# Optimization experiments

Hardware: AMD Instinct MI355X
Metric: run time of the kernel (lower is better)

## Reference

```python
import jax, jax.numpy as jnp
import numpy as np

N, D, K, G = 262144, 256, 1024, 4
C = D // G
BETA = 0.5


def setup_inputs() -> dict:
    key = jax.random.key(0)
    k1, k2 = jax.random.split(key)
    z = jax.random.normal(k1, (N, D), dtype=jnp.float32)
    # original init: uniform(-1/K, 1/K)
    codebooks = jax.random.uniform(k2, (G, K, C), dtype=jnp.float32,
                                   minval=-1.0 / K, maxval=1.0 / K)
    return {"z": z, "codebooks": codebooks}


def reference(z, codebooks):
    # z: [N, D] -> [N, G, C]; codebooks: [G, K, C]
    zg = z.reshape(-1, G, C)
    # squared distances: ||z||^2 + ||e||^2 - 2 z.e  -> [N, G, K]
    z_sq = jnp.sum(zg ** 2, axis=-1, keepdims=True)            # [N, G, 1]
    e_sq = jnp.sum(codebooks ** 2, axis=-1)                    # [G, K]
    dots = jnp.einsum('ngc,gkc->ngk', zg, codebooks)           # [N, G, K]
    d = z_sq + e_sq[None, :, :] - 2.0 * dots
    idx = jnp.argmin(d, axis=-1)                               # [N, G]
    # gather codes: [N, G, C]
    zq = codebooks[jnp.arange(G)[None, :], idx]
    # per-group VQ loss, averaged over groups (means over N and C per group)
    sg = jax.lax.stop_gradient
    commit = jnp.mean((sg(zq) - zg) ** 2, axis=(0, 2))         # [G]
    embed = jnp.mean((zq - sg(zg)) ** 2, axis=(0, 2))          # [G]
    loss = jnp.mean(BETA * commit + embed)
    # straight-through estimator
    zq_st = zg + sg(zq - zg)
    return zq_st.reshape(-1, D), loss
```

## Files before the change

kernel.cpp:

```cpp
#include <hip/hip_runtime.h>
#include <hip/hip_fp16.h>
#include <stdint.h>

typedef _Float16 f16;
typedef f16   f16x8 __attribute__((ext_vector_type(8)));
typedef float f32x4 __attribute__((ext_vector_type(4)));

#define NTOK 262144
#define DDIM 256
#define KCB  1024
#define GG   4
#define CC   64
#define FR   4
#define WAVES 16
#define ROWS_PER_BLK (FR * 16 * WAVES)
#define NBLKX (NTOK / ROWS_PER_BLK)
#define NPART (NBLKX * GG)
#define CBB   (KCB * CC * 2)

static __device__ __forceinline__ uint32_t umin32(uint32_t a, uint32_t b) { return a < b ? a : b; }

typedef __attribute__((address_space(1))) const void gv_t;
typedef __attribute__((address_space(3))) void lv_t;
static __device__ __forceinline__ void gl_lds16(const void* g, void* l) {
    __builtin_amdgcn_global_load_lds((gv_t*)g, (lv_t*)l, 16, 0, 0);
}
static __device__ __forceinline__ void gl_lds4(const void* g, void* l) {
    __builtin_amdgcn_global_load_lds((gv_t*)g, (lv_t*)l, 4, 0, 0);
}

__global__ __launch_bounds__(64) void vq_prep(const float* __restrict__ cb,
                                              f16* __restrict__ cb16,
                                              float* __restrict__ esq05) {
    int gk = blockIdx.x;
    int c  = threadIdx.x;
    float v = cb[(size_t)gk * CC + c];
    cb16[(size_t)gk * CC + c] = (f16)v;
    float s = v * v;
    #pragma unroll
    for (int off = 32; off; off >>= 1) s += __shfl_down(s, off, 64);
    if (c == 0) esq05[gk] = 0.5f + s;
}

__global__ __launch_bounds__(1024, 4) void vq_argmin(const float* __restrict__ z,
                                                     const f16* __restrict__ cb16,
                                                     const float* __restrict__ esq05,
                                                     unsigned short* __restrict__ idx,
                                                     float* __restrict__ part) {
    const int tid  = threadIdx.x;
    const int lane = tid & 63;
    const int w    = tid >> 6;
    const int g    = blockIdx.y;
    const int r0   = blockIdx.x * ROWS_PER_BLK + w * (FR * 16);
    const int q    = lane >> 4;
    const int t    = lane & 15;

    __shared__ __align__(16) char sb[CBB + KCB * 4];
    __shared__ float ls[WAVES];

    const f16*   cbg = cb16  + (size_t)g * KCB * CC;
    const float* eg  = esq05 + (size_t)g * KCB;

    #pragma unroll
    for (int c = 0; c < 8; ++c) {
        uint32_t x  = (uint32_t)(c * 16384 + w * 1024 + lane * 16);
        uint32_t gx = x ^ (((x >> 7) & 7u) << 4);
        gl_lds16((const char*)cbg + gx, &sb[c * 16384 + w * 1024]);
    }
    gl_lds4(eg + tid, &sb[CBB + w * 256]);

    f16x8 a[FR][2];
    float zsq[FR];
    #pragma unroll
    for (int f = 0; f < FR; ++f) {
        int row = r0 + f * 16 + t;
        const float* zp = z + (size_t)row * DDIM + g * CC + q * 8;
        float4 v0 = *(const float4*)(zp);
        float4 v1 = *(const float4*)(zp + 4);
        float4 v2 = *(const float4*)(zp + 32);
        float4 v3 = *(const float4*)(zp + 36);
        f16x8 a0 = { (f16)(-2.f*v0.x),(f16)(-2.f*v0.y),(f16)(-2.f*v0.z),(f16)(-2.f*v0.w),
                     (f16)(-2.f*v1.x),(f16)(-2.f*v1.y),(f16)(-2.f*v1.z),(f16)(-2.f*v1.w) };
        f16x8 a1 = { (f16)(-2.f*v2.x),(f16)(-2.f*v2.y),(f16)(-2.f*v2.z),(f16)(-2.f*v2.w),
                     (f16)(-2.f*v3.x),(f16)(-2.f*v3.y),(f16)(-2.f*v3.z),(f16)(-2.f*v3.w) };
        a[f][0] = a0; a[f][1] = a1;
        float s = v0.x*v0.x + v0.y*v0.y + v0.z*v0.z + v0.w*v0.w
                + v1.x*v1.x + v1.y*v1.y + v1.z*v1.z + v1.w*v1.w
                + v2.x*v2.x + v2.y*v2.y + v2.z*v2.z + v2.w*v2.w
                + v3.x*v3.x + v3.y*v3.y + v3.z*v3.z + v3.w*v3.w;
        s += __shfl_xor(s, 16, 64);
        s += __shfl_xor(s, 32, 64);
        zsq[f] = s;
    }

    uint32_t run[FR][4];
    #pragma unroll
    for (int f = 0; f < FR; ++f)
        #pragma unroll
        for (int i = 0; i < 4; ++i) run[f][i] = 0xFFFFFFFFu;

    const uint32_t binner = (uint32_t)t * 128 + (((uint32_t)(q * 16)) ^ (((uint32_t)(t & 7)) << 4));

    __syncthreads();

    const float* eb = (const float*)(sb + CBB);

    #pragma unroll 2
    for (int s = 0; s < 64; s += 2) {
        const char* pA = sb + (size_t)s * 2048;
        f16x8 b0A = *(const f16x8*)(pA + binner);
        f16x8 b1A = *(const f16x8*)(pA + (binner ^ 64));
        f16x8 b0B = *(const f16x8*)(pA + 2048 + binner);
        f16x8 b1B = *(const f16x8*)(pA + 2048 + (binner ^ 64));
        float eA = eb[s * 16 + t];
        float eB = eb[s * 16 + 16 + t];
        f32x4 ceA = { eA, eA, eA, eA };
        f32x4 ceB = { eB, eB, eB, eB };
        uint32_t codeA = (uint32_t)(s * 16 + t);
        __builtin_amdgcn_s_setprio(1);
        #pragma unroll
        for (int f = 0; f < FR; ++f) {
            f32x4 accA = __builtin_amdgcn_mfma_f32_16x16x32_f16(a[f][0], b0A, ceA, 0, 0, 0);
            accA = __builtin_amdgcn_mfma_f32_16x16x32_f16(a[f][1], b1A, accA, 0, 0, 0);
            f32x4 accB = __builtin_amdgcn_mfma_f32_16x16x32_f16(a[f][0], b0B, ceB, 0, 0, 0);
            accB = __builtin_amdgcn_mfma_f32_16x16x32_f16(a[f][1], b1B, accB, 0, 0, 0);
            #pragma unroll
            for (int i = 0; i < 4; ++i) {
                uint32_t kA = (__float_as_uint(accA[i]) & 0xFFFFFC00u) | codeA;
                uint32_t kB = (__float_as_uint(accB[i]) & 0xFFFFFC00u) | (codeA + 16);
                run[f][i] = umin32(run[f][i], umin32(kA, kB));
            }
        }
        __builtin_amdgcn_s_setprio(0);
    }

    float lsum = 0.0f;
    #pragma unroll
    for (int f = 0; f < FR; ++f) {
        #pragma unroll
        for (int i = 0; i < 4; ++i) {
            uint32_t k = run[f][i];
            k = umin32(k, __shfl_xor(k, 1, 64));
            k = umin32(k, __shfl_xor(k, 2, 64));
            k = umin32(k, __shfl_xor(k, 4, 64));
            k = umin32(k, __shfl_xor(k, 8, 64));
            int   kw     = (int)(k & 1023u);
            float minval = __uint_as_float(k & 0xFFFFFC00u) - 0.5f;
            int rloc = q * 4 + i;
            int grow = r0 + f * 16 + rloc;
            float zs = __shfl(zsq[f], rloc, 64);
            if (t == 0) {
                idx[(grow << 2) | g] = (unsigned short)kw;
                lsum += zs + minval;
            }
        }
    }
    #pragma unroll
    for (int off = 32; off; off >>= 1) lsum += __shfl_down(lsum, off, 64);

    if (lane == 0) ls[w] = lsum;
    __syncthreads();
    if (tid == 0) {
        float s = 0.0f;
        #pragma unroll
        for (int i = 0; i < WAVES; ++i) s += ls[i];
        part[blockIdx.y * NBLKX + blockIdx.x] = s;
    }
}

__global__ __launch_bounds__(256) void vq_gather(const unsigned short* __restrict__ idx,
                                                 const float* __restrict__ cb32,
                                                 float* __restrict__ out) {
    const int stride = gridDim.x * 256;
    const int total  = NTOK * (DDIM / 4);
    for (int i = blockIdx.x * 256 + threadIdx.x; i < total; i += stride) {
        int row = i >> 6;
        int d4  = i & 63;
        int g   = d4 >> 4;
        int c4  = d4 & 15;
        int k   = idx[(row << 2) | g];
        float4 v = *(const float4*)(cb32 + (size_t)(((g << 10) + k) << 6) + (c4 << 2));
        *(float4*)(out + ((size_t)row << 8) + (d4 << 2)) = v;
    }
}

__global__ __launch_bounds__(256) void vq_final(const float* __restrict__ part,
                                                float* __restrict__ out_loss) {
    __shared__ float ls[4];
    float s = 0.0f;
    for (int i = threadIdx.x; i < NPART; i += 256) s += part[i];
    #pragma unroll
    for (int off = 32; off; off >>= 1) s += __shfl_down(s, off, 64);
    int lane = threadIdx.x & 63, w = threadIdx.x >> 6;
    if (lane == 0) ls[w] = s;
    __syncthreads();
    if (threadIdx.x == 0) {
        *out_loss = 1.5f * (ls[0] + ls[1] + ls[2] + ls[3]) * (1.0f / ((float)NTOK * (float)DDIM));
    }
}

extern "C" void kernel_launch(void* const* d_in, const int* in_sizes, int n_in,
                              void* d_out, int out_size, void* d_ws, size_t ws_size,
                              hipStream_t stream) {
    const float* z  = (const float*)d_in[0];
    const float* cb = (const float*)d_in[1];
    float* out = (float*)d_out;

    char* ws = (char*)d_ws;
    f16*   cb16  = (f16*)ws;
    float* esq05 = (float*)(ws + (size_t)GG * KCB * CC * sizeof(f16));
    float* part  = (float*)(ws + 512*1024 + 16*1024);
    unsigned short* idx = (unsigned short*)(ws + 512*1024 + 32*1024);

    vq_prep<<<GG * KCB, 64, 0, stream>>>(cb, cb16, esq05);

    dim3 grid(NBLKX, GG);
    vq_argmin<<<grid, 1024, 0, stream>>>(z, cb16, esq05, idx, part);

    vq_gather<<<4096, 256, 0, stream>>>(idx, cb, out);

    vq_final<<<1, 256, 0, stream>>>(part, out + (size_t)NTOK * DDIM);
}
```

Before: 272.8 us.

## Switch argmin distance MFMA from fp16 to scaled fp8 32x32x64

Both the codebook (prescaled by 1024) and -2*z are quantized to fp8, and the distance dot products use the MI355X scaled MFMA 32x32x64 f8f6f4 instruction, with a block scale that undoes the codebook prescale. The block shrinks to 8 waves of 64 rows each, the LDS codebook footprint halves, and the reduction is adjusted to the 32-wide tile layout. The aim is higher matrix throughput and less LDS traffic in the argmin kernel. The cost is much coarser fp8 precision, which can flip argmin choices between near-tied codes and change the loss.

Result: faster. 251.7 us (-7.7%).

```diff
diff --git a/kernel.cpp b/kernel.cpp
--- a/kernel.cpp
+++ b/kernel.cpp
@@ -1,22 +1,20 @@
 #include <hip/hip_runtime.h>
-#include <hip/hip_fp16.h>
 #include <stdint.h>
 
-typedef _Float16 f16;
-typedef f16   f16x8 __attribute__((ext_vector_type(8)));
-typedef float f32x4 __attribute__((ext_vector_type(4)));
+typedef int   i32x4 __attribute__((ext_vector_type(4)));
+typedef int   i32x8 __attribute__((ext_vector_type(8)));
+typedef float f32x16 __attribute__((ext_vector_type(16)));
 
 #define NTOK 262144
 #define DDIM 256
 #define KCB  1024
 #define GG   4
 #define CC   64
-#define FR   4
-#define WAVES 16
-#define ROWS_PER_BLK (FR * 16 * WAVES)
+#define WAVES 8
+#define ROWS_PER_BLK (WAVES * 64)
 #define NBLKX (NTOK / ROWS_PER_BLK)
 #define NPART (NBLKX * GG)
-#define CBB   (KCB * CC * 2)
+#define CB8B  (KCB * CC)
 
 static __device__ __forceinline__ uint32_t umin32(uint32_t a, uint32_t b) { return a < b ? a : b; }
 
@@ -30,126 +28,141 @@
 }
 
 __global__ __launch_bounds__(64) void vq_prep(const float* __restrict__ cb,
-                                              f16* __restrict__ cb16,
+                                              unsigned short* __restrict__ cb8,
                                               float* __restrict__ esq05) {
     int gk = blockIdx.x;
     int c  = threadIdx.x;
     float v = cb[(size_t)gk * CC + c];
-    cb16[(size_t)gk * CC + c] = (f16)v;
     float s = v * v;
     #pragma unroll
     for (int off = 32; off; off >>= 1) s += __shfl_down(s, off, 64);
     if (c == 0) esq05[gk] = 0.5f + s;
-}
-
-__global__ __launch_bounds__(1024, 4) void vq_argmin(const float* __restrict__ z,
-                                                     const f16* __restrict__ cb16,
-                                                     const float* __restrict__ esq05,
-                                                     unsigned short* __restrict__ idx,
-                                                     float* __restrict__ part) {
+    if (c < 32) {
+        float v0 = cb[(size_t)gk * CC + 2 * c]     * 1024.0f;
+        float v1 = cb[(size_t)gk * CC + 2 * c + 1] * 1024.0f;
+        int p = __builtin_amdgcn_cvt_pk_fp8_f32(v0, v1, 0, false);
+        cb8[gk * 32 + c] = (unsigned short)(p & 0xFFFF);
+    }
+}
+
+__global__ __launch_bounds__(512, 4) void vq_argmin(const float* __restrict__ z,
+                                                    const unsigned char* __restrict__ cb8,
+                                                    const float* __restrict__ esq05,
+                                                    unsigned short* __restrict__ idx,
+                                                    float* __restrict__ part) {
     const int tid  = threadIdx.x;
     const int lane = tid & 63;
     const int w    = tid >> 6;
     const int g    = blockIdx.y;
-    const int r0   = blockIdx.x * ROWS_PER_BLK + w * (FR * 16);
-    const int q    = lane >> 4;
-    const int t    = lane & 15;
-
-    __shared__ __align__(16) char sb[CBB + KCB * 4];
+    const int r0   = blockIdx.x * ROWS_PER_BLK + w * 64;
+    const int c5   = lane & 31;
+    const int h    = lane >> 5;
+
+    __shared__ __align__(16) char sb[CB8B + KCB * 4];
     __shared__ float ls[WAVES];
 
-    const f16*   cbg = cb16  + (size_t)g * KCB * CC;
-    const float* eg  = esq05 + (size_t)g * KCB;
-
-    #pragma unroll
-    for (int c = 0; c < 8; ++c) {
-        uint32_t x  = (uint32_t)(c * 16384 + w * 1024 + lane * 16);
-        uint32_t gx = x ^ (((x >> 7) & 7u) << 4);
-        gl_lds16((const char*)cbg + gx, &sb[c * 16384 + w * 1024]);
-    }
-    gl_lds4(eg + tid, &sb[CBB + w * 256]);
-
-    f16x8 a[FR][2];
-    float zsq[FR];
-    #pragma unroll
-    for (int f = 0; f < FR; ++f) {
-        int row = r0 + f * 16 + t;
-        const float* zp = z + (size_t)row * DDIM + g * CC + q * 8;
-        float4 v0 = *(const float4*)(zp);
-        float4 v1 = *(const float4*)(zp + 4);
-        float4 v2 = *(const float4*)(zp + 32);
-        float4 v3 = *(const float4*)(zp + 36);
-        f16x8 a0 = { (f16)(-2.f*v0.x),(f16)(-2.f*v0.y),(f16)(-2.f*v0.z),(f16)(-2.f*v0.w),
-                     (f16)(-2.f*v1.x),(f16)(-2.f*v1.y),(f16)(-2.f*v1.z),(f16)(-2.f*v1.w) };
-        f16x8 a1 = { (f16)(-2.f*v2.x),(f16)(-2.f*v2.y),(f16)(-2.f*v2.z),(f16)(-2.f*v2.w),
-                     (f16)(-2.f*v3.x),(f16)(-2.f*v3.y),(f16)(-2.f*v3.z),(f16)(-2.f*v3.w) };
-        a[f][0] = a0; a[f][1] = a1;
-        float s = v0.x*v0.x + v0.y*v0.y + v0.z*v0.z + v0.w*v0.w
-                + v1.x*v1.x + v1.y*v1.y + v1.z*v1.z + v1.w*v1.w
-                + v2.x*v2.x + v2.y*v2.y + v2.z*v2.z + v2.w*v2.w
-                + v3.x*v3.x + v3.y*v3.y + v3.z*v3.z + v3.w*v3.w;
-        s += __shfl_xor(s, 16, 64);
+    const unsigned char* cbg8 = cb8 + (size_t)g * CB8B;
+    const float*         eg   = esq05 + (size_t)g * KCB;
+
+    #pragma unroll
+    for (int i8 = 0; i8 < 8; ++i8) {
+        int i = w + 8 * i8;
+        int s = i >> 1, slot = i & 1;
+        const unsigned char* src = cbg8 + ((s * 32 + c5) * CC + h * 32 + slot * 16);
+        gl_lds16(src, &sb[i * 1024]);
+    }
+    gl_lds4(eg + w * 64 + lane,       &sb[CB8B + w * 256]);
+    gl_lds4(eg + 512 + w * 64 + lane, &sb[CB8B + 2048 + w * 256]);
+
+    i32x8 a[2];
+    float zsq[2];
+    #pragma unroll
+    for (int f = 0; f < 2; ++f) {
+        const float* zp = z + (size_t)(r0 + f * 32 + c5) * DDIM + g * CC + h * 32;
+        int w8[8];
+        float s = 0.0f;
+        #pragma unroll
+        for (int j = 0; j < 8; ++j) {
+            float4 v = ((const float4*)zp)[j];
+            s += v.x * v.x + v.y * v.y + v.z * v.z + v.w * v.w;
+            int p = __builtin_amdgcn_cvt_pk_fp8_f32(-2.0f * v.x, -2.0f * v.y, 0, false);
+            p     = __builtin_amdgcn_cvt_pk_fp8_f32(-2.0f * v.z, -2.0f * v.w, p, true);
+            w8[j] = p;
+        }
+        a[f] = (i32x8){w8[0], w8[1], w8[2], w8[3], w8[4], w8[5], w8[6], w8[7]};
         s += __shfl_xor(s, 32, 64);
         zsq[f] = s;
     }
 
-    uint32_t run[FR][4];
-    #pragma unroll
-    for (int f = 0; f < FR; ++f)
-        #pragma unroll
-        for (int i = 0; i < 4; ++i) run[f][i] = 0xFFFFFFFFu;
-
-    const uint32_t binner = (uint32_t)t * 128 + (((uint32_t)(q * 16)) ^ (((uint32_t)(t & 7)) << 4));
+    uint32_t run[2][16];
+    #pragma unroll
+    for (int f = 0; f < 2; ++f)
+        #pragma unroll
+        for (int r = 0; r < 16; ++r) run[f][r] = 0xFFFFFFFFu;
 
     __syncthreads();
 
-    const float* eb = (const float*)(sb + CBB);
-
-    #pragma unroll 2
-    for (int s = 0; s < 64; s += 2) {
-        const char* pA = sb + (size_t)s * 2048;
-        f16x8 b0A = *(const f16x8*)(pA + binner);
-        f16x8 b1A = *(const f16x8*)(pA + (binner ^ 64));
-        f16x8 b0B = *(const f16x8*)(pA + 2048 + binner);
-        f16x8 b1B = *(const f16x8*)(pA + 2048 + (binner ^ 64));
-        float eA = eb[s * 16 + t];
-        float eB = eb[s * 16 + 16 + t];
-        f32x4 ceA = { eA, eA, eA, eA };
-        f32x4 ceB = { eB, eB, eB, eB };
-        uint32_t codeA = (uint32_t)(s * 16 + t);
+    const float* eb = (const float*)(sb + CB8B);
+
+    #pragma unroll 1
+    for (int s2 = 0; s2 < 32; s2 += 2) {
+        const char* p0 = sb + (size_t)s2 * 2048;
+        i32x4 aLo = *(const i32x4*)(p0 + lane * 16);
+        i32x4 aHi = *(const i32x4*)(p0 + 1024 + lane * 16);
+        i32x4 bLo = *(const i32x4*)(p0 + 2048 + lane * 16);
+        i32x4 bHi = *(const i32x4*)(p0 + 3072 + lane * 16);
+        i32x8 bA = (i32x8){aLo[0], aLo[1], aLo[2], aLo[3], aHi[0], aHi[1], aHi[2], aHi[3]};
+        i32x8 bB = (i32x8){bLo[0], bLo[1], bLo[2], bLo[3], bHi[0], bHi[1], bHi[2], bHi[3]};
+        float eA = eb[s2 * 32 + c5];
+        float eB = eb[s2 * 32 + 32 + c5];
+        f32x16 ceA, ceB;
+        #pragma unroll
+        for (int i = 0; i < 16; ++i) { ceA[i] = eA; ceB[i] = eB; }
+        uint32_t codeA = (uint32_t)(s2 * 32 + c5);
+
         __builtin_amdgcn_s_setprio(1);
-        #pragma unroll
-        for (int f = 0; f < FR; ++f) {
-            f32x4 accA = __builtin_amdgcn_mfma_f32_16x16x32_f16(a[f][0], b0A, ceA, 0, 0, 0);
-            accA = __builtin_amdgcn_mfma_f32_16x16x32_f16(a[f][1], b1A, accA, 0, 0, 0);
-            f32x4 accB = __builtin_amdgcn_mfma_f32_16x16x32_f16(a[f][0], b0B, ceB, 0, 0, 0);
-            accB = __builtin_amdgcn_mfma_f32_16x16x32_f16(a[f][1], b1B, accB, 0, 0, 0);
-            #pragma unroll
-            for (int i = 0; i < 4; ++i) {
-                uint32_t kA = (__float_as_uint(accA[i]) & 0xFFFFFC00u) | codeA;
-                uint32_t kB = (__float_as_uint(accB[i]) & 0xFFFFFC00u) | (codeA + 16);
-                run[f][i] = umin32(run[f][i], umin32(kA, kB));
-            }
-        }
+        f32x16 acc00 = __builtin_amdgcn_mfma_scale_f32_32x32x64_f8f6f4(
+            a[0], bA, ceA, 0, 0, 0, 0x7F7F7F7F, 0, 0x75757575);
+        f32x16 acc01 = __builtin_amdgcn_mfma_scale_f32_32x32x64_f8f6f4(
+            a[0], bB, ceB, 0, 0, 0, 0x7F7F7F7F, 0, 0x75757575);
         __builtin_amdgcn_s_setprio(0);
+        #pragma unroll
+        for (int r = 0; r < 16; ++r) {
+            uint32_t kA = (__float_as_uint(acc00[r]) & 0xFFFFFC00u) | codeA;
+            uint32_t kB = (__float_as_uint(acc01[r]) & 0xFFFFFC00u) | (codeA + 32u);
+            run[0][r] = umin32(run[0][r], umin32(kA, kB));
+        }
+        __builtin_amdgcn_s_setprio(1);
+        f32x16 acc10 = __builtin_amdgcn_mfma_scale_f32_32x32x64_f8f6f4(
+            a[1], bA, ceA, 0, 0, 0, 0x7F7F7F7F, 0, 0x75757575);
+        f32x16 acc11 = __builtin_amdgcn_mfma_scale_f32_32x32x64_f8f6f4(
+            a[1], bB, ceB, 0, 0, 0, 0x7F7F7F7F, 0, 0x75757575);
+        __builtin_amdgcn_s_setprio(0);
+        #pragma unroll
+        for (int r = 0; r < 16; ++r) {
+            uint32_t kA = (__float_as_uint(acc10[r]) & 0xFFFFFC00u) | codeA;
+            uint32_t kB = (__float_as_uint(acc11[r]) & 0xFFFFFC00u) | (codeA + 32u);
+            run[1][r] = umin32(run[1][r], umin32(kA, kB));
+        }
     }
 
     float lsum = 0.0f;
     #pragma unroll
-    for (int f = 0; f < FR; ++f) {
-        #pragma unroll
-        for (int i = 0; i < 4; ++i) {
-            uint32_t k = run[f][i];
+    for (int f = 0; f < 2; ++f) {
+        #pragma unroll
+        for (int r = 0; r < 16; ++r) {
+            uint32_t k = run[f][r];
             k = umin32(k, __shfl_xor(k, 1, 64));
             k = umin32(k, __shfl_xor(k, 2, 64));
             k = umin32(k, __shfl_xor(k, 4, 64));
             k = umin32(k, __shfl_xor(k, 8, 64));
+            k = umin32(k, __shfl_xor(k, 16, 64));
             int   kw     = (int)(k & 1023u);
             float minval = __uint_as_float(k & 0xFFFFFC00u) - 0.5f;
-            int rloc = q * 4 + i;
-            int grow = r0 + f * 16 + rloc;
+            int rloc = (r & 3) + 8 * (r >> 2) + 4 * h;
+            int grow = r0 + f * 32 + rloc;
             float zs = __shfl(zsq[f], rloc, 64);
-            if (t == 0) {
+            if (c5 == 0) {
                 idx[(grow << 2) | g] = (unsigned short)kw;
                 lsum += zs + minval;
             }
@@ -207,15 +220,15 @@
     float* out = (float*)d_out;
 
     char* ws = (char*)d_ws;
-    f16*   cb16  = (f16*)ws;
-    float* esq05 = (float*)(ws + (size_t)GG * KCB * CC * sizeof(f16));
-    float* part  = (float*)(ws + 512*1024 + 16*1024);
-    unsigned short* idx = (unsigned short*)(ws + 512*1024 + 32*1024);
-
-    vq_prep<<<GG * KCB, 64, 0, stream>>>(cb, cb16, esq05);
+    unsigned short* cb8 = (unsigned short*)ws;
+    float* esq05 = (float*)(ws + 256 * 1024);
+    float* part  = (float*)(ws + 256 * 1024 + 16 * 1024);
+    unsigned short* idx = (unsigned short*)(ws + 256 * 1024 + 32 * 1024);
+
+    vq_prep<<<GG * KCB, 64, 0, stream>>>(cb, cb8, esq05);
 
     dim3 grid(NBLKX, GG);
-    vq_argmin<<<grid, 1024, 0, stream>>>(z, cb16, esq05, idx, part);
+    vq_argmin<<<grid, 512, 0, stream>>>(z, (const unsigned char*)cb8, esq05, idx, part);
 
     vq_gather<<<4096, 256, 0, stream>>>(idx, cb, out);
 
```

## Stage codebook in two halves with 512-thread blocks and register prefetch

Applied to the files above, without the earlier changes.

The argmin kernel now uses 8-wave blocks and loads the codebook into LDS in two 512-code halves instead of all 1024 codes at once. This roughly halves LDS per block so more blocks can be resident. The LDS layout is rearranged into a fragment-ordered, conflict-free form, and the next step's B fragments are prefetched into registers. The cost is an extra barrier and reload per block, with the second-half load no longer overlapped, and s_setprio hints are dropped.

New measurement: 244.5 us. 10.4% less time.

```diff
diff --git a/kernel.cpp b/kernel.cpp
--- a/kernel.cpp
+++ b/kernel.cpp
@@ -11,12 +11,13 @@
 #define KCB  1024
 #define GG   4
 #define CC   64
+#define WAVES 8
 #define FR   4
-#define WAVES 16
-#define ROWS_PER_BLK (FR * 16 * WAVES)
+#define ROWS_PER_BLK (WAVES * FR * 16)
 #define NBLKX (NTOK / ROWS_PER_BLK)
 #define NPART (NBLKX * GG)
-#define CBB   (KCB * CC * 2)
+#define KHALF 512
+#define CBH   (KHALF * CC * 2)
 
 static __device__ __forceinline__ uint32_t umin32(uint32_t a, uint32_t b) { return a < b ? a : b; }
 
@@ -42,11 +43,11 @@
     if (c == 0) esq05[gk] = 0.5f + s;
 }
 
-__global__ __launch_bounds__(1024, 4) void vq_argmin(const float* __restrict__ z,
-                                                     const f16* __restrict__ cb16,
-                                                     const float* __restrict__ esq05,
-                                                     unsigned short* __restrict__ idx,
-                                                     float* __restrict__ part) {
+__global__ __launch_bounds__(512, 4) void vq_argmin(const float* __restrict__ z,
+                                                    const f16* __restrict__ cb16,
+                                                    const float* __restrict__ esq05,
+                                                    unsigned short* __restrict__ idx,
+                                                    float* __restrict__ part) {
     const int tid  = threadIdx.x;
     const int lane = tid & 63;
     const int w    = tid >> 6;
@@ -55,19 +56,26 @@
     const int q    = lane >> 4;
     const int t    = lane & 15;
 
-    __shared__ __align__(16) char sb[CBB + KCB * 4];
+    __shared__ __align__(16) char sb[CBH + KHALF * 4];
     __shared__ float ls[WAVES];
 
     const f16*   cbg = cb16  + (size_t)g * KCB * CC;
     const float* eg  = esq05 + (size_t)g * KCB;
 
-    #pragma unroll
-    for (int c = 0; c < 8; ++c) {
-        uint32_t x  = (uint32_t)(c * 16384 + w * 1024 + lane * 16);
-        uint32_t gx = x ^ (((x >> 7) & 7u) << 4);
-        gl_lds16((const char*)cbg + gx, &sb[c * 16384 + w * 1024]);
-    }
-    gl_lds4(eg + tid, &sb[CBB + w * 256]);
+    #define STAGE(ph)                                                                 \
+        do {                                                                          \
+            _Pragma("unroll")                                                         \
+            for (int j = 0; j < 8; ++j) {                                             \
+                int c  = w + 8 * j;                                                   \
+                int s  = c >> 1, hf = c & 1;                                          \
+                const f16* src = cbg + ((size_t)((ph) * KHALF + s * 16 + t) * CC      \
+                                        + hf * 32 + q * 8);                           \
+                gl_lds16(src, &sb[c * 1024]);                                         \
+            }                                                                         \
+            gl_lds4(eg + (ph) * KHALF + tid, &sb[CBH + w * 256]);                     \
+        } while (0)
+
+    STAGE(0);
 
     f16x8 a[FR][2];
     float zsq[FR];
@@ -99,39 +107,48 @@
         #pragma unroll
         for (int i = 0; i < 4; ++i) run[f][i] = 0xFFFFFFFFu;
 
-    const uint32_t binner = (uint32_t)t * 128 + (((uint32_t)(q * 16)) ^ (((uint32_t)(t & 7)) << 4));
-
-    __syncthreads();
-
-    const float* eb = (const float*)(sb + CBB);
-
-    #pragma unroll 2
-    for (int s = 0; s < 64; s += 2) {
-        const char* pA = sb + (size_t)s * 2048;
-        f16x8 b0A = *(const f16x8*)(pA + binner);
-        f16x8 b1A = *(const f16x8*)(pA + (binner ^ 64));
-        f16x8 b0B = *(const f16x8*)(pA + 2048 + binner);
-        f16x8 b1B = *(const f16x8*)(pA + 2048 + (binner ^ 64));
-        float eA = eb[s * 16 + t];
-        float eB = eb[s * 16 + 16 + t];
-        f32x4 ceA = { eA, eA, eA, eA };
-        f32x4 ceB = { eB, eB, eB, eB };
-        uint32_t codeA = (uint32_t)(s * 16 + t);
-        __builtin_amdgcn_s_setprio(1);
-        #pragma unroll
-        for (int f = 0; f < FR; ++f) {
-            f32x4 accA = __builtin_amdgcn_mfma_f32_16x16x32_f16(a[f][0], b0A, ceA, 0, 0, 0);
-            accA = __builtin_amdgcn_mfma_f32_16x16x32_f16(a[f][1], b1A, accA, 0, 0, 0);
-            f32x4 accB = __builtin_amdgcn_mfma_f32_16x16x32_f16(a[f][0], b0B, ceB, 0, 0, 0);
-            accB = __builtin_amdgcn_mfma_f32_16x16x32_f16(a[f][1], b1B, accB, 0, 0, 0);
+    const float* eb = (const float*)(sb + CBH);
+
+    #pragma unroll 1
+    for (int ph = 0; ph < 2; ++ph) {
+        __syncthreads();
+        f16x8 c0 = *(const f16x8*)(sb + lane * 16);
+        f16x8 c1 = *(const f16x8*)(sb + 1024 + lane * 16);
+        f16x8 c2 = *(const f16x8*)(sb + 2048 + lane * 16);
+        f16x8 c3 = *(const f16x8*)(sb + 3072 + lane * 16);
+        #pragma unroll 1
+        for (int s2 = 0; s2 < 32; s2 += 2) {
+            int ns = (s2 + 2) & 31;
+            const char* pn = sb + (size_t)ns * 2048;
+            f16x8 n0 = *(const f16x8*)(pn + lane * 16);
+            f16x8 n1 = *(const f16x8*)(pn + 1024 + lane * 16);
+            f16x8 n2 = *(const f16x8*)(pn + 2048 + lane * 16);
+            f16x8 n3 = *(const f16x8*)(pn + 3072 + lane * 16);
+
+            float eA = eb[s2 * 16 + t];
+            float eB = eb[s2 * 16 + 16 + t];
+            f32x4 ceA = { eA, eA, eA, eA };
+            f32x4 ceB = { eB, eB, eB, eB };
+            uint32_t codeA = (uint32_t)(ph * KHALF + s2 * 16 + t);
             #pragma unroll
-            for (int i = 0; i < 4; ++i) {
-                uint32_t kA = (__float_as_uint(accA[i]) & 0xFFFFFC00u) | codeA;
-                uint32_t kB = (__float_as_uint(accB[i]) & 0xFFFFFC00u) | (codeA + 16);
-                run[f][i] = umin32(run[f][i], umin32(kA, kB));
+            for (int f = 0; f < FR; ++f) {
+                f32x4 accA = __builtin_amdgcn_mfma_f32_16x16x32_f16(a[f][0], c0, ceA, 0, 0, 0);
+                accA = __builtin_amdgcn_mfma_f32_16x16x32_f16(a[f][1], c1, accA, 0, 0, 0);
+                f32x4 accB = __builtin_amdgcn_mfma_f32_16x16x32_f16(a[f][0], c2, ceB, 0, 0, 0);
+                accB = __builtin_amdgcn_mfma_f32_16x16x32_f16(a[f][1], c3, accB, 0, 0, 0);
+                #pragma unroll
+                for (int i = 0; i < 4; ++i) {
+                    uint32_t kA = (__float_as_uint(accA[i]) & 0xFFFFFC00u) | codeA;
+                    uint32_t kB = (__float_as_uint(accB[i]) & 0xFFFFFC00u) | (codeA + 16);
+                    run[f][i] = umin32(run[f][i], umin32(kA, kB));
+                }
             }
+            c0 = n0; c1 = n1; c2 = n2; c3 = n3;
         }
-        __builtin_amdgcn_s_setprio(0);
+        if (ph == 0) {
+            __syncthreads();
+            STAGE(1);
+        }
     }
 
     float lsum = 0.0f;
@@ -208,14 +225,14 @@
 
     char* ws = (char*)d_ws;
     f16*   cb16  = (f16*)ws;
-    float* esq05 = (float*)(ws + (size_t)GG * KCB * CC * sizeof(f16));
-    float* part  = (float*)(ws + 512*1024 + 16*1024);
-    unsigned short* idx = (unsigned short*)(ws + 512*1024 + 32*1024);
+    float* esq05 = (float*)(ws + 512 * 1024);
+    float* part  = (float*)(ws + 512 * 1024 + 16 * 1024);
+    unsigned short* idx = (unsigned short*)(ws + 512 * 1024 + 32 * 1024);
 
     vq_prep<<<GG * KCB, 64, 0, stream>>>(cb, cb16, esq05);
 
     dim3 grid(NBLKX, GG);
-    vq_argmin<<<grid, 1024, 0, stream>>>(z, cb16, esq05, idx, part);
+    vq_argmin<<<grid, 512, 0, stream>>>(z, cb16, esq05, idx, part);
 
     vq_gather<<<4096, 256, 0, stream>>>(idx, cb, out);
 
```
